# Kernel optimization log

Hardware: AMD Instinct MI355X
Metric: run time of the kernel (lower is better)

The kernel has to match this reference:

```python
import jax, jax.numpy as jnp
import numpy as np

B, G, D_EMB = 4096, 20000, 512
H_LOW, N_HIDDEN = 512, 1024
TOPK, T, FILM_W = 64, 0.1, 1.0
LN_EPS = 1e-5


def _layer_norm(x, gamma, beta):
    mu = jnp.mean(x, axis=-1, keepdims=True)
    var = jnp.mean(jnp.square(x - mu), axis=-1, keepdims=True)
    return (x - mu) * jax.lax.rsqrt(var + LN_EPS) * gamma + beta


def _l2norm(x, eps=1e-12):
    n = jnp.sqrt(jnp.sum(jnp.square(x), axis=-1, keepdims=True))
    return x / jnp.maximum(n, eps)


def setup_inputs() -> dict:
    key = jax.random.key(0)
    ks = jax.random.split(key, 8)
    s = 0.02
    return {
        "x": jax.random.normal(ks[0], (B, G), jnp.float32),
        "g": jax.random.normal(ks[1], (G, D_EMB), jnp.float32),
        "W_enc": jax.random.normal(ks[2], (H_LOW, G), jnp.float32) * s,
        "b_enc": jnp.zeros((H_LOW,), jnp.float32),
        "ln1_g": jnp.ones((H_LOW,), jnp.float32),
        "ln1_b": jnp.zeros((H_LOW,), jnp.float32),
        "W_ga": jax.random.normal(ks[3], (H_LOW, D_EMB), jnp.float32) * s,
        "W_gamma": jax.random.normal(ks[4], (H_LOW, H_LOW), jnp.float32) * s,
        "b_gamma": jnp.zeros((H_LOW,), jnp.float32),
        "W_beta": jax.random.normal(ks[5], (H_LOW, H_LOW), jnp.float32) * s,
        "b_beta": jnp.zeros((H_LOW,), jnp.float32),
        "W_exp": jax.random.normal(ks[6], (N_HIDDEN, H_LOW), jnp.float32) * s,
        "b_exp": jnp.zeros((N_HIDDEN,), jnp.float32),
        "ln2_g": jnp.ones((N_HIDDEN,), jnp.float32),
        "ln2_b": jnp.zeros((N_HIDDEN,), jnp.float32),
    }


def reference(x, g, W_enc, b_enc, ln1_g, ln1_b, W_ga, W_gamma, b_gamma,
              W_beta, b_beta, W_exp, b_exp, ln2_g, ln2_b):
    # x_encoder: Linear -> LayerNorm -> GELU (dropout = eval no-op)
    h = jnp.dot(x, W_enc.T) + b_enc                    # [B, H_LOW]
    h = jax.nn.gelu(_layer_norm(h, ln1_g, ln1_b), approximate=False)
    # gene adapter + cosine scores
    e = _l2norm(jnp.dot(g, W_ga.T))                    # [G, H_LOW]
    h_x = _l2norm(h)                                   # [B, H_LOW]
    scores = jnp.dot(h_x, e.T) / T                     # [B, G]
    # top-k mask + masked softmax attention
    _, idx = jax.lax.top_k(scores, TOPK)               # [B, TOPK]
    mask = jnp.zeros_like(scores).at[jnp.arange(B)[:, None], idx].set(1.0)
    attn = jax.nn.softmax(jnp.where(mask == 0, -1e9, scores), axis=-1)
    ctx = jnp.dot(attn, e)                             # [B, H_LOW]
    # FiLM (identity-centered)
    gamma = (jnp.dot(ctx, W_gamma.T) + b_gamma) * FILM_W
    beta = (jnp.dot(ctx, W_beta.T) + b_beta) * FILM_W
    h_cell = (1.0 + gamma) * h_x + beta
    # x_expand: Linear -> LayerNorm -> GELU
    h2 = jnp.dot(h_cell, W_exp.T) + b_exp              # [B, N_HIDDEN]
    return jax.nn.gelu(_layer_norm(h2, ln2_g, ln2_b), approximate=False)
```

## Files before the change

### kernel.cpp

```cpp
#include <hip/hip_runtime.h>
#include <hip/hip_fp16.h>
#include <math.h>
#include <type_traits>

#define DEVI __device__ __forceinline__

typedef __attribute__((ext_vector_type(8))) short bf16x8;
typedef __attribute__((ext_vector_type(4))) float f32x4;
typedef __attribute__((ext_vector_type(4))) unsigned int u32x4;
typedef unsigned short ushort_t;

DEVI unsigned int pack_bf16(float a, float b) {
  unsigned int ua = __float_as_uint(a), ub = __float_as_uint(b);
  ua = (ua + 0x7FFFu + ((ua >> 16) & 1u)) >> 16;
  ub = (ub + 0x7FFFu + ((ub >> 16) & 1u)) >> 16;
  return ua | (ub << 16);
}

DEVI ushort_t rnd_bf16(float a) {
  unsigned int ua = __float_as_uint(a);
  return (ushort_t)((ua + 0x7FFFu + ((ua >> 16) & 1u)) >> 16);
}

DEVI bf16x8 cvt_bf16x8(f32x4 lo, f32x4 hi) {
  unsigned int r0, r1, r2, r3;
  asm("v_cvt_pk_bf16_f32 %0, %1, %2" : "=v"(r0) : "v"(lo[0]), "v"(lo[1]));
  asm("v_cvt_pk_bf16_f32 %0, %1, %2" : "=v"(r1) : "v"(lo[2]), "v"(lo[3]));
  asm("v_cvt_pk_bf16_f32 %0, %1, %2" : "=v"(r2) : "v"(hi[0]), "v"(hi[1]));
  asm("v_cvt_pk_bf16_f32 %0, %1, %2" : "=v"(r3) : "v"(hi[2]), "v"(hi[3]));
  union { u32x4 u; bf16x8 v; } x;
  x.u = u32x4{r0, r1, r2, r3};
  return x.v;
}

template<int SPLITZ, bool TAIL>
__global__ __launch_bounds__(512, 1) void bgemmA32(
    const float* __restrict__ A, const ushort_t* __restrict__ B,
    float* __restrict__ C, int M, int N, int K, int nbn, int nbm)
{
  __shared__ __align__(16) char L[131072];
  const int tid = threadIdx.x, lane = tid & 63, wv = tid >> 6;

  const int nwg = gridDim.x;
  const int hw = blockIdx.x;
  const int q = nwg >> 3, r = nwg & 7;
  const int xcd = hw & 7, pos = hw >> 3;
  const int lid = (xcd < r ? xcd * (q + 1) : r * (q + 1) + (xcd - r) * q) + pos;
  const int bn = lid % nbn;
  const int t2 = lid / nbn;
  const int bm = t2 % nbm;
  const int z  = t2 / nbm;

  const int ksteps = K >> 6;
  const int szk = (ksteps + SPLITZ - 1) / SPLITZ;
  const int kbBeg = z * szk;
  const int kbEnd = min(ksteps, kbBeg + szk);

  const int wm = wv >> 2, wn = wv & 3;
  const int lrow = lane & 15, kg = lane >> 4;

  f32x4 acc[4][4];
#pragma unroll
  for (int i = 0; i < 4; ++i)
#pragma unroll
    for (int j = 0; j < 4; ++j) acc[i][j] = f32x4{0.f, 0.f, 0.f, 0.f};

  const int alr = lane >> 3, ag32 = (lane & 7) >> 1;
  const float* aS[2];
#pragma unroll
  for (int j = 0; j < 2; ++j) {
    const int lr = (wv * 2 + j) * 8 + alr;
    const int swz = (lr ^ (lr >> 2)) & 3;
    const int colf = ((ag32 ^ swz) << 3) + (lane & 1) * 4;
    aS[j] = A + (size_t)min(bm * 128 + lr, M - 1) * (size_t)K + colf;
  }
  const int blr = lane >> 2, bgq = lane & 3;
  const ushort_t* bS[2];
#pragma unroll
  for (int j = 0; j < 2; ++j) {
    const int lr = (wv * 2 + j) * 16 + blr;
    const int swz = (lr ^ (lr >> 2)) & 3;
    bS[j] = B + (size_t)min(bn * 256 + lr, N - 1) * (size_t)K + ((bgq ^ swz) << 3);
  }

  int offA[4], offB[4];
#pragma unroll
  for (int i = 0; i < 4; ++i) {
    const int ra = wm * 64 + i * 16 + lrow;
    offA[i] = ra * 128 + ((kg ^ ((ra ^ (ra >> 2)) & 3)) << 5);
  }
#pragma unroll
  for (int j = 0; j < 4; ++j) {
    const int rb = wn * 64 + j * 16 + lrow;
    offB[j] = rb * 64 + ((kg ^ ((rb ^ (rb >> 2)) & 3)) << 4);
  }

#define GA_STGA(h, k0v) do {                                                  \
    _Pragma("unroll")                                                         \
    for (int j_ = 0; j_ < 2; ++j_)                                            \
      __builtin_amdgcn_global_load_lds(                                       \
          (const __attribute__((address_space(1))) void*)(aS[j_] + (k0v) + (h) * 32), \
          (__attribute__((address_space(3))) void*)                           \
              (L + (s ^ 1) * 32768 + (h) * 16384 + (wv * 2 + j_) * 1024),     \
          16, 0, 0);                                                          \
  } while (0)
#define GA_STGB(h, k0v) do {                                                  \
    _Pragma("unroll")                                                         \
    for (int j_ = 0; j_ < 2; ++j_)                                            \
      __builtin_amdgcn_global_load_lds(                                       \
          (const __attribute__((address_space(1))) void*)(bS[j_] + (k0v) + (h) * 32), \
          (__attribute__((address_space(3))) void*)                           \
              (L + 65536 + (s ^ 1) * 32768 + (h) * 16384 + (wv * 2 + j_) * 1024), \
          16, 0, 0);                                                          \
  } while (0)
#define GA_RDB(h) do {                                                        \
    _Pragma("unroll")                                                         \
    for (int j_ = 0; j_ < 4; ++j_)                                            \
      bfv[j_] = *(const bf16x8*)(L + 65536 + s * 32768 + (h) * 16384 + offB[j_]); \
  } while (0)
#define GA_RDA(h, rg) do {                                                    \
    _Pragma("unroll")                                                         \
    for (int i_ = 0; i_ < 2; ++i_) {                                          \
      const char* pa_ = L + s * 32768 + (h) * 16384 + offA[(rg) * 2 + i_];    \
      af[i_] = cvt_bf16x8(*(const f32x4*)pa_, *(const f32x4*)(pa_ + 16));     \
    }                                                                         \
  } while (0)
#define GA_MM(rg) do {                                                        \
    _Pragma("unroll")                                                         \
    for (int i_ = 0; i_ < 2; ++i_)                                            \
      _Pragma("unroll")                                                       \
      for (int j_ = 0; j_ < 4; ++j_)                                          \
        acc[(rg) * 2 + i_][j_] = __builtin_amdgcn_mfma_f32_16x16x32_bf16(     \
            af[i_], bfv[j_], acc[(rg) * 2 + i_][j_], 0, 0, 0);                \
  } while (0)
#define GA_BAR asm volatile("s_barrier" ::: "memory")

  {
    int s = 1;
    const int k0 = kbBeg << 6;
    GA_STGA(0, k0); GA_STGB(0, k0); GA_STGA(1, k0); GA_STGB(1, k0);
  }
  asm volatile("s_waitcnt vmcnt(4)" ::: "memory");
  GA_BAR;

  int s = 0;
  for (int t = kbBeg; t < kbEnd; ++t) {
    const bool more = (t + 1 < kbEnd);
    const int k0n = (t + 1) << 6;
    bf16x8 af[2], bfv[4];
    GA_RDB(0); GA_RDA(0, 0);
    if (more) GA_STGA(0, k0n);
    GA_BAR;
    __builtin_amdgcn_s_setprio(1); GA_MM(0); __builtin_amdgcn_s_setprio(0);
    GA_BAR;
    GA_RDA(0, 1);
    if (more) GA_STGB(0, k0n);
    GA_BAR;
    __builtin_amdgcn_s_setprio(1); GA_MM(1); __builtin_amdgcn_s_setprio(0);
    if (more) asm volatile("s_waitcnt vmcnt(4)" ::: "memory");
    else      asm volatile("s_waitcnt vmcnt(0)" ::: "memory");
    GA_BAR;
    GA_RDB(1); GA_RDA(1, 0);
    if (more) GA_STGA(1, k0n);
    GA_BAR;
    __builtin_amdgcn_s_setprio(1); GA_MM(0); __builtin_amdgcn_s_setprio(0);
    GA_BAR;
    GA_RDA(1, 1);
    if (more) GA_STGB(1, k0n);
    GA_BAR;
    __builtin_amdgcn_s_setprio(1); GA_MM(1); __builtin_amdgcn_s_setprio(0);
    if (more) asm volatile("s_waitcnt vmcnt(4)" ::: "memory");
    GA_BAR;
    s ^= 1;
  }

  if (TAIL && z == SPLITZ - 1 && (K & 63)) {
    const int k0t = ksteps << 6;
    bf16x8 af[2], bfv[4];
#pragma unroll
    for (int j = 0; j < 2; ++j) {
      const float4 av = *(const float4*)(aS[j] + k0t);
      *(float4*)(L + s * 32768 + (wv * 2 + j) * 1024 + lane * 16) = av;
      const u32x4 bv = *(const u32x4*)(bS[j] + k0t);
      *(u32x4*)(L + 65536 + s * 32768 + (wv * 2 + j) * 1024 + lane * 16) = bv;
    }
    __syncthreads();
    GA_RDB(0);
    GA_RDA(0, 0); GA_MM(0);
    GA_RDA(0, 1); GA_MM(1);
  }
#undef GA_STGA
#undef GA_STGB
#undef GA_RDB
#undef GA_RDA
#undef GA_MM
#undef GA_BAR

  const size_t zoff = (SPLITZ > 1) ? (size_t)z * (size_t)M * (size_t)N : 0;
#pragma unroll
  for (int i = 0; i < 4; ++i) {
#pragma unroll
    for (int j = 0; j < 4; ++j) {
      const int col = bn * 256 + wn * 64 + j * 16 + lrow;
      if (col >= N) continue;
      const int row0 = bm * 128 + wm * 64 + i * 16 + kg * 4;
#pragma unroll
      for (int rr = 0; rr < 4; ++rr) {
        const int gr = row0 + rr;
        if (gr < M) C[zoff + (size_t)gr * (size_t)N + col] = acc[i][j][rr];
      }
    }
  }
}

template<int SPLITZ, typename OutT>
__global__ __launch_bounds__(512, 1) void bgemm256(
    const ushort_t* __restrict__ A, const ushort_t* __restrict__ B,
    OutT* __restrict__ C, int M, int N, int K, int nbn, int nbm)
{
  __shared__ __align__(16) char L[131072];
  const int tid = threadIdx.x, lane = tid & 63, wv = tid >> 6;

  const int nwg = gridDim.x;
  const int hw = blockIdx.x;
  const int q = nwg >> 3, r = nwg & 7;
  const int xcd = hw & 7, pos = hw >> 3;
  const int lid = (xcd < r ? xcd * (q + 1) : r * (q + 1) + (xcd - r) * q) + pos;
  const int bn = lid % nbn;
  const int t2 = lid / nbn;
  const int bm = t2 % nbm;
  const int z  = t2 / nbm;

  const int ksteps = K >> 6;
  int kbBeg = 0, kbEnd = ksteps;
  if (SPLITZ > 1) {
    const int sz = (ksteps + SPLITZ - 1) / SPLITZ;
    kbBeg = z * sz;
    kbEnd = min(ksteps, kbBeg + sz);
  }

  const int wm = wv >> 2, wn = wv & 3;
  const int lrow = lane & 15, kg = lane >> 4;

  f32x4 acc[8][4];
#pragma unroll
  for (int i = 0; i < 8; ++i)
#pragma unroll
    for (int j = 0; j < 4; ++j) acc[i][j] = f32x4{0.f, 0.f, 0.f, 0.f};

  const int sr = lane >> 2, sq = lane & 3;
  const ushort_t* aS[2];
  const ushort_t* bS[2];
#pragma unroll
  for (int j = 0; j < 2; ++j) {
    const int lr = (wv * 2 + j) * 16 + sr;
    const int swz = (lr ^ (lr >> 2)) & 3;
    aS[j] = A + (size_t)min(bm * 256 + lr, M - 1) * (size_t)K + ((sq ^ swz) << 3);
    bS[j] = B + (size_t)min(bn * 256 + lr, N - 1) * (size_t)K + ((sq ^ swz) << 3);
  }

  int offA[8], offB[4];
#pragma unroll
  for (int i = 0; i < 8; ++i) {
    const int ra = wm * 128 + i * 16 + lrow;
    offA[i] = ra * 64 + (((kg ^ ((ra ^ (ra >> 2)) & 3))) << 4);
  }
#pragma unroll
  for (int j = 0; j < 4; ++j) {
    const int rb = wn * 64 + j * 16 + lrow;
    offB[j] = rb * 64 + (((kg ^ ((rb ^ (rb >> 2)) & 3))) << 4);
  }

#define G256_STG(isB, h, k0v) do {                                            \
    _Pragma("unroll")                                                         \
    for (int j_ = 0; j_ < 2; ++j_)                                            \
      __builtin_amdgcn_global_load_lds(                                       \
          (const __attribute__((address_space(1))) void*)                     \
              (((isB) ? bS : aS)[j_] + (k0v) + (h) * 32),                     \
          (__attribute__((address_space(3))) void*)                           \
              (L + (isB) * 65536 + (s ^ 1) * 32768 + (h) * 16384 +            \
               (wv * 2 + j_) * 1024), 16, 0, 0);                              \
  } while (0)
#define G256_RDA(h, rg) do {                                                  \
    _Pragma("unroll")                                                         \
    for (int i_ = 0; i_ < 4; ++i_)                                            \
      af[i_] = *(const bf16x8*)(L + s * 32768 + (h) * 16384 +                 \
                                offA[(rg) * 4 + i_]);                         \
  } while (0)
#define G256_RDB(h) do {                                                      \
    _Pragma("unroll")                                                         \
    for (int j_ = 0; j_ < 4; ++j_)                                            \
      bfv[j_] = *(const bf16x8*)(L + 65536 + s * 32768 + (h) * 16384 +        \
                                 offB[j_]);                                   \
  } while (0)
#define G256_MM(rg) do {                                                      \
    _Pragma("unroll")                                                         \
    for (int i_ = 0; i_ < 4; ++i_)                                            \
      _Pragma("unroll")                                                       \
      for (int j_ = 0; j_ < 4; ++j_)                                          \
        acc[(rg) * 4 + i_][j_] = __builtin_amdgcn_mfma_f32_16x16x32_bf16(     \
            af[i_], bfv[j_], acc[(rg) * 4 + i_][j_], 0, 0, 0);                \
  } while (0)
#define G256_BAR asm volatile("s_barrier" ::: "memory")

  {
    int s = 1;
    const int k0 = kbBeg << 6;
    G256_STG(0, 0, k0);
    G256_STG(1, 0, k0);
    G256_STG(0, 1, k0);
    G256_STG(1, 1, k0);
  }
  asm volatile("s_waitcnt vmcnt(4)" ::: "memory");
  G256_BAR;

  int s = 0;
  for (int t = kbBeg; t < kbEnd; ++t) {
    const bool more = (t + 1 < kbEnd);
    const int k0n = (t + 1) << 6;
    bf16x8 af[4], bfv[4];
    G256_RDB(0);
    G256_RDA(0, 0);
    if (more) G256_STG(0, 0, k0n);
    G256_BAR;
    __builtin_amdgcn_s_setprio(1); G256_MM(0); __builtin_amdgcn_s_setprio(0);
    G256_BAR;
    G256_RDA(0, 1);
    if (more) G256_STG(1, 0, k0n);
    G256_BAR;
    __builtin_amdgcn_s_setprio(1); G256_MM(1); __builtin_amdgcn_s_setprio(0);
    if (more) asm volatile("s_waitcnt vmcnt(4)" ::: "memory");
    else      asm volatile("s_waitcnt vmcnt(0)" ::: "memory");
    G256_BAR;
    G256_RDB(1);
    G256_RDA(1, 0);
    if (more) G256_STG(0, 1, k0n);
    G256_BAR;
    __builtin_amdgcn_s_setprio(1); G256_MM(0); __builtin_amdgcn_s_setprio(0);
    G256_BAR;
    G256_RDA(1, 1);
    if (more) G256_STG(1, 1, k0n);
    G256_BAR;
    __builtin_amdgcn_s_setprio(1); G256_MM(1); __builtin_amdgcn_s_setprio(0);
    if (more) asm volatile("s_waitcnt vmcnt(4)" ::: "memory");
    G256_BAR;
    s ^= 1;
  }
#undef G256_STG
#undef G256_RDA
#undef G256_RDB
#undef G256_MM
#undef G256_BAR

  const size_t zoff = (SPLITZ > 1) ? (size_t)z * (size_t)M * (size_t)N : 0;
#pragma unroll
  for (int i = 0; i < 8; ++i) {
#pragma unroll
    for (int j = 0; j < 4; ++j) {
      const int col = bn * 256 + wn * 64 + j * 16 + lrow;
      if (col >= N) continue;
      const int row0 = bm * 256 + wm * 128 + i * 16 + kg * 4;
#pragma unroll
      for (int rr = 0; rr < 4; ++rr) {
        const int gr = row0 + rr;
        if (gr < M) {
          const float v = acc[i][j][rr];
          if constexpr (std::is_same<OutT, __half>::value)
            C[zoff + (size_t)gr * (size_t)N + col] = __float2half(v);
          else
            C[zoff + (size_t)gr * (size_t)N + col] = v;
        }
      }
    }
  }
}

template<typename AT, int SPLITZ, bool BIAS, typename OutT>
__global__ __launch_bounds__(512, sizeof(AT) == 2 ? 3 : 2) void bgemm(
    const AT* __restrict__ A, const ushort_t* __restrict__ B0,
    const float* __restrict__ bias0, OutT* __restrict__ C,
    int M, int N, int K, int nbn, int nbm)
{
  constexpr bool AB16 = (sizeof(AT) == 2);
  __shared__ __align__(16) char AsB[AB16 ? 16384 : 32768];
  __shared__ __align__(16) char BsB[32768];
  const int tid = threadIdx.x, lane = tid & 63, wv = tid >> 6;

  const int nwg = gridDim.x;
  const int hw = blockIdx.x;
  const int q = nwg >> 3, r = nwg & 7;
  const int xcd = hw & 7, pos = hw >> 3;
  const int lid = (xcd < r ? xcd * (q + 1) : r * (q + 1) + (xcd - r) * q) + pos;
  const int bn = lid % nbn;
  const int t2 = lid / nbn;
  const int bm = t2 % nbm;
  const int z  = t2 / nbm;

  const ushort_t* B  = B0;
  const float* bias  = bias0;

  const int ksteps = (K + 63) >> 6;
  int kbBeg = 0, kbEnd = ksteps;
  if (SPLITZ > 1) {
    const int sz = (ksteps + SPLITZ - 1) / SPLITZ;
    kbBeg = z * sz;
    kbEnd = min(ksteps, kbBeg + sz);
  }

  const int wr = (wv >> 2) * 64;
  const int wc = (wv & 3) * 64;
  const int lrow = lane & 15, kg = lane >> 4;

  f32x4 acc[4][4];
#pragma unroll
  for (int i = 0; i < 4; ++i)
#pragma unroll
    for (int j = 0; j < 4; ++j) acc[i][j] = f32x4{0.f, 0.f, 0.f, 0.f};

  const AT* aSrc[4];
  if constexpr (AB16) {
    const int r0 = lane >> 3;
    const int ce = ((lane & 7) ^ r0) << 3;
#pragma unroll
    for (int j = 0; j < 2; ++j) {
      const int row = wv * 16 + j * 8 + r0;
      aSrc[j] = A + (size_t)min(bm * 128 + row, M - 1) * (size_t)K + ce;
    }
  } else {
    const int r0 = lane >> 4;
#pragma unroll
    for (int j = 0; j < 4; ++j) {
      const int row = wv * 16 + j * 4 + r0;
      const int ca = ((lane & 15) << 2) ^ ((row & 7) << 3);
      aSrc[j] = A + (size_t)min(bm * 128 + row, M - 1) * (size_t)K + ca;
    }
  }
  const int rB0 = lane >> 3;
  const int colB = ((lane & 7) ^ rB0) << 3;
  const ushort_t* bSrc[4];
#pragma unroll
  for (int j = 0; j < 4; ++j) {
    const int row = wv * 32 + j * 8 + rB0;
    bSrc[j] = B + (size_t)min(bn * 256 + row, N - 1) * (size_t)K + colB;
  }

  for (int kb = kbBeg; kb < kbEnd; ++kb) {
    const int k0 = kb << 6;
    if constexpr (AB16) {
#pragma unroll
      for (int j = 0; j < 2; ++j)
        __builtin_amdgcn_global_load_lds(
            (const __attribute__((address_space(1))) void*)(aSrc[j] + k0),
            (__attribute__((address_space(3))) void*)(AsB + (wv * 2 + j) * 1024),
            16, 0, 0);
    } else {
#pragma unroll
      for (int j = 0; j < 4; ++j)
        __builtin_amdgcn_global_load_lds(
            (const __attribute__((address_space(1))) void*)(aSrc[j] + k0),
            (__attribute__((address_space(3))) void*)(AsB + (wv * 4 + j) * 1024),
            16, 0, 0);
    }
#pragma unroll
    for (int j = 0; j < 4; ++j)
      __builtin_amdgcn_global_load_lds(
          (const __attribute__((address_space(1))) void*)(bSrc[j] + k0),
          (__attribute__((address_space(3))) void*)(BsB + (wv * 4 + j) * 1024),
          16, 0, 0);
    __syncthreads();
#pragma unroll
    for (int kk = 0; kk < 2; ++kk) {
      bf16x8 af[4], bfr[4];
#pragma unroll
      for (int i = 0; i < 4; ++i) {
        const int ra = wr + i * 16 + lrow;
        if constexpr (AB16) {
          af[i] = *(const bf16x8*)(AsB + ra * 128 + ((((kk << 2) + kg) ^ (ra & 7)) << 4));
        } else {
          const char* pa = AsB + ra * 256 + ((kk * 128 + (kg << 5)) ^ ((ra & 7) << 5));
          af[i] = cvt_bf16x8(*(const f32x4*)pa, *(const f32x4*)(pa + 16));
        }
        const int rb = wc + i * 16 + lrow;
        bfr[i] = *(const bf16x8*)(BsB + rb * 128 + ((((kk << 2) + kg) ^ (rb & 7)) << 4));
      }
#pragma unroll
      for (int i = 0; i < 4; ++i)
#pragma unroll
        for (int j = 0; j < 4; ++j)
          acc[i][j] = __builtin_amdgcn_mfma_f32_16x16x32_bf16(af[i], bfr[j], acc[i][j], 0, 0, 0);
    }
    __syncthreads();
  }

  const size_t zoff = (SPLITZ > 1) ? (size_t)z * (size_t)M * (size_t)N : 0;
#pragma unroll
  for (int i = 0; i < 4; ++i) {
#pragma unroll
    for (int j = 0; j < 4; ++j) {
      const int col = bn * 256 + wc + j * 16 + lrow;
      if (col >= N) continue;
      const int row0 = bm * 128 + wr + i * 16 + kg * 4;
      float bv = 0.f;
      if (BIAS) bv = bias[col];
#pragma unroll
      for (int rr = 0; rr < 4; ++rr) {
        const int gr = row0 + rr;
        if (gr < M) {
          const float v = acc[i][j][rr] + bv;
          if constexpr (std::is_same<OutT, __half>::value)
            C[zoff + (size_t)gr * (size_t)N + col] = __float2half(v);
          else
            C[zoff + (size_t)gr * (size_t)N + col] = v;
        }
      }
    }
  }
}

__global__ __launch_bounds__(512, 2) void bgemm_film(
    const ushort_t* __restrict__ A, const ushort_t* __restrict__ BG,
    const ushort_t* __restrict__ BB, const float* __restrict__ bg,
    const float* __restrict__ bb, const float* __restrict__ hx,
    ushort_t* __restrict__ hcb)
{
  constexpr int M = 4096, N = 512, K = 512;
  __shared__ __align__(16) char AsB[16384];
  __shared__ __align__(16) char BsB[65536];
  const int tid = threadIdx.x, lane = tid & 63, wv = tid >> 6;

  const int nwg = gridDim.x;
  const int hw = blockIdx.x;
  const int q = nwg >> 3, r = nwg & 7;
  const int xcd = hw & 7, pos = hw >> 3;
  const int lid = (xcd < r ? xcd * (q + 1) : r * (q + 1) + (xcd - r) * q) + pos;
  const int bn = lid % 2;
  const int bm = lid / 2;

  const int wr = (wv >> 2) * 64;
  const int wc = (wv & 3) * 64;
  const int lrow = lane & 15, kg = lane >> 4;

  f32x4 accG[4][4], accB[4][4];
#pragma unroll
  for (int i = 0; i < 4; ++i)
#pragma unroll
    for (int j = 0; j < 4; ++j) {
      accG[i][j] = f32x4{0.f, 0.f, 0.f, 0.f};
      accB[i][j] = f32x4{0.f, 0.f, 0.f, 0.f};
    }

  const int r0 = lane >> 3;
  const int ce = ((lane & 7) ^ r0) << 3;
  const ushort_t* aSrc[2];
#pragma unroll
  for (int j = 0; j < 2; ++j) {
    const int row = wv * 16 + j * 8 + r0;
    aSrc[j] = A + (size_t)(bm * 128 + row) * (size_t)K + ce;
  }
  const ushort_t* gSrc[4];
  const ushort_t* bSrc[4];
#pragma unroll
  for (int j = 0; j < 4; ++j) {
    const int row = wv * 32 + j * 8 + r0;
    gSrc[j] = BG + (size_t)(bn * 256 + row) * (size_t)K + ce;
    bSrc[j] = BB + (size_t)(bn * 256 + row) * (size_t)K + ce;
  }

  for (int kb = 0; kb < K / 64; ++kb) {
    const int k0 = kb << 6;
#pragma unroll
    for (int j = 0; j < 2; ++j)
      __builtin_amdgcn_global_load_lds(
          (const __attribute__((address_space(1))) void*)(aSrc[j] + k0),
          (__attribute__((address_space(3))) void*)(AsB + (wv * 2 + j) * 1024),
          16, 0, 0);
#pragma unroll
    for (int j = 0; j < 4; ++j) {
      __builtin_amdgcn_global_load_lds(
          (const __attribute__((address_space(1))) void*)(gSrc[j] + k0),
          (__attribute__((address_space(3))) void*)(BsB + (wv * 4 + j) * 1024),
          16, 0, 0);
      __builtin_amdgcn_global_load_lds(
          (const __attribute__((address_space(1))) void*)(bSrc[j] + k0),
          (__attribute__((address_space(3))) void*)(BsB + 32768 + (wv * 4 + j) * 1024),
          16, 0, 0);
    }
    __syncthreads();
#pragma unroll
    for (int kk = 0; kk < 2; ++kk) {
      bf16x8 af[4], bfG[4], bfB[4];
#pragma unroll
      for (int i = 0; i < 4; ++i) {
        const int ra = wr + i * 16 + lrow;
        af[i] = *(const bf16x8*)(AsB + ra * 128 + ((((kk << 2) + kg) ^ (ra & 7)) << 4));
        const int rb = wc + i * 16 + lrow;
        const int bo = rb * 128 + ((((kk << 2) + kg) ^ (rb & 7)) << 4);
        bfG[i] = *(const bf16x8*)(BsB + bo);
        bfB[i] = *(const bf16x8*)(BsB + 32768 + bo);
      }
#pragma unroll
      for (int i = 0; i < 4; ++i)
#pragma unroll
        for (int j = 0; j < 4; ++j) {
          accG[i][j] = __builtin_amdgcn_mfma_f32_16x16x32_bf16(af[i], bfG[j], accG[i][j], 0, 0, 0);
          accB[i][j] = __builtin_amdgcn_mfma_f32_16x16x32_bf16(af[i], bfB[j], accB[i][j], 0, 0, 0);
        }
    }
    __syncthreads();
  }

#pragma unroll
  for (int i = 0; i < 4; ++i) {
#pragma unroll
    for (int j = 0; j < 4; ++j) {
      const int col = bn * 256 + wc + j * 16 + lrow;
      const float gvb = bg[col], bvb = bb[col];
      const int row0 = bm * 128 + wr + i * 16 + kg * 4;
#pragma unroll
      for (int rr = 0; rr < 4; ++rr) {
        const int gr = row0 + rr;
        const float gm = accG[i][j][rr] + gvb;
        const float bt = accB[i][j][rr] + bvb;
        const float h = hx[(size_t)gr * N + col];
        hcb[(size_t)gr * N + col] = rnd_bf16((1.f + gm) * h + bt);
      }
    }
  }
}

__global__ __launch_bounds__(256) void f2b(
    const float4* __restrict__ in, u32x4* __restrict__ out, int n8)
{
  const int i = blockIdx.x * 256 + threadIdx.x;
  if (i < n8) {
    const float4 a = in[2 * i], b = in[2 * i + 1];
    u32x4 o = { pack_bf16(a.x, a.y), pack_bf16(a.z, a.w),
                pack_bf16(b.x, b.y), pack_bf16(b.z, b.w) };
    out[i] = o;
  }
}

__global__ __launch_bounds__(256) void gee_fuse_ln1(
    const float* __restrict__ P, const float* __restrict__ b_enc,
    const float* __restrict__ g1, const float* __restrict__ b1,
    float* __restrict__ hx, unsigned int* __restrict__ hxb)
{
  const int row = blockIdx.x, tid = threadIdx.x;
  __shared__ float red[16];
  const size_t MN = (size_t)4096 * 512;
  const size_t o2 = (size_t)row * 256 + tid;
  float2 v = ((const float2*)b_enc)[tid];
#pragma unroll
  for (int qq = 0; qq < 4; ++qq) {
    const float2 p = ((const float2*)P)[qq * (MN / 2) + o2];
    v.x += p.x; v.y += p.y;
  }
  float a = v.x + v.y;
  float b = v.x * v.x + v.y * v.y;
#pragma unroll
  for (int o = 32; o > 0; o >>= 1) { a += __shfl_xor(a, o); b += __shfl_xor(b, o); }
  const int lane = tid & 63, wvi = tid >> 6;
  if (lane == 0) { red[wvi] = a; red[8 + wvi] = b; }
  __syncthreads();
  const float mu  = (red[0] + red[1] + red[2] + red[3]) * (1.f / 512.f);
  const float ex2 = (red[8] + red[9] + red[10] + red[11]) * (1.f / 512.f);
  const float inv = rsqrtf(ex2 - mu * mu + 1e-5f);
  const float2 gg = ((const float2*)g1)[tid];
  const float2 bb = ((const float2*)b1)[tid];
  const float y0 = (v.x - mu) * inv * gg.x + bb.x;
  const float y1 = (v.y - mu) * inv * gg.y + bb.y;
  const float t0 = 0.5f * y0 * (1.f + erff(y0 * 0.70710678118654752f));
  const float t1 = 0.5f * y1 * (1.f + erff(y1 * 0.70710678118654752f));
  float ss = t0 * t0 + t1 * t1;
  __syncthreads();
#pragma unroll
  for (int o = 32; o > 0; o >>= 1) ss += __shfl_xor(ss, o);
  if (lane == 0) red[wvi] = ss;
  __syncthreads();
  const float sc = 1.f / fmaxf(sqrtf(red[0] + red[1] + red[2] + red[3]), 1e-12f);
  const float h0 = t0 * sc, h1 = t1 * sc;
  ((float2*)hx)[o2] = make_float2(h0, h1);
  hxb[o2] = pack_bf16(h0, h1);
}

__global__ __launch_bounds__(256) void gee_l2rows(
    const __half2* __restrict__ ein, unsigned int* __restrict__ eb)
{
  const int row = blockIdx.x, tid = threadIdx.x;
  __shared__ float red[4];
  const __half2 h = ein[(size_t)row * 256 + tid];
  const float vx = __half2float(h.x), vy = __half2float(h.y);
  float ss = vx * vx + vy * vy;
#pragma unroll
  for (int o = 32; o > 0; o >>= 1) ss += __shfl_xor(ss, o);
  if ((tid & 63) == 0) red[tid >> 6] = ss;
  __syncthreads();
  const float sc = 1.f / fmaxf(sqrtf(red[0] + red[1] + red[2] + red[3]), 1e-12f);
  eb[(size_t)row * 256 + tid] = pack_bf16(vx * sc, vy * sc);
}

__global__ __launch_bounds__(256) void gee_topk_ctx(
    const __half* __restrict__ scores, const unsigned int* __restrict__ eb,
    unsigned int* __restrict__ ctxb)
{
  constexpr int G = 20000, GQ = G / 8, CAP = 2048, TCAP = 160;
  constexpr unsigned int SPEC = 0xADu;
  const int row = blockIdx.x, tid = threadIdx.x;
  const int lane = tid & 63, wv = tid >> 6;
  __shared__ int hist[4][256];
  __shared__ int cnt_ge[256];
  __shared__ int wtop[4];
  __shared__ unsigned int comp[CAP];
  __shared__ int whist[4][16];
  __shared__ int sel[64];
  __shared__ float swt[64];
  __shared__ int tie[TCAP];
  __shared__ int s_thr, s_above, s_cand, s_cnt, s_n1, s_n2;

  const u32x4* srow128 = (const u32x4*)((const ushort_t*)scores + (size_t)row * G);
  const ushort_t* srow16 = (const ushort_t*)srow128;

#pragma unroll
  for (int b = 0; b < 4; ++b) hist[b][tid] = 0;
  if (tid == 0) { s_cnt = 0; s_n1 = 0; s_n2 = 0; }
  __syncthreads();

  for (int j0 = 0; j0 < GQ; j0 += 256) {
    const int j = j0 + tid;
    if (j < GQ) {
      const u32x4 pv = srow128[j];
#pragma unroll
      for (int c = 0; c < 4; ++c) {
        const unsigned int p = pv[c];
        const unsigned int f = (((p >> 15) & 0x10001u) * 0x7FFFu) + 0x80008000u;
        const unsigned int k2 = p ^ f;
        const unsigned int bl = (k2 >> 8) & 0xFFu, bh = k2 >> 24;
        atomicAdd(&hist[wv][bl], 1);
        atomicAdd(&hist[wv][bh], 1);
        if (bl >= SPEC) {
          const int pp = atomicAdd(&s_cnt, 1);
          if (pp < CAP) comp[pp] = ((k2 & 0xFFFFu) << 16) | (unsigned)(8 * j + 2 * c);
        }
        if (bh >= SPEC) {
          const int pp = atomicAdd(&s_cnt, 1);
          if (pp < CAP) comp[pp] = ((k2 >> 16) << 16) | (unsigned)(8 * j + 2 * c + 1);
        }
      }
    }
  }
  __syncthreads();
  cnt_ge[tid] = hist[0][tid] + hist[1][tid] + hist[2][tid] + hist[3][tid];
  __syncthreads();
  for (int off = 1; off < 256; off <<= 1) {
    const int add = (tid + off < 256) ? cnt_ge[tid + off] : 0;
    __syncthreads();
    cnt_ge[tid] += add;
    __syncthreads();
  }
  {
    const unsigned long long m = __ballot(cnt_ge[tid] >= 64);
    if (lane == 0) wtop[wv] = m ? (wv * 64 + 63 - __clzll(m)) : -1;
  }
  __syncthreads();
  if (tid == 0) {
    const int thrB = max(max(wtop[0], wtop[1]), max(wtop[2], wtop[3]));
    s_cand  = cnt_ge[thrB];
    s_above = (thrB == 255) ? 0 : cnt_ge[thrB + 1];
    s_thr   = thrB << 8;
  }
  __syncthreads();

  const unsigned int thrB = ((unsigned int)s_thr) >> 8;
  const int specCnt = cnt_ge[SPEC];
  const bool useSpec = (thrB >= SPEC) && (specCnt <= CAP);
  const bool useComp = useSpec || (s_cand <= CAP);

  if (!useSpec && useComp) {
    __syncthreads();
    if (tid == 0) s_cnt = 0;
    __syncthreads();
    for (int j0 = 0; j0 < GQ; j0 += 256) {
      const int j = j0 + tid;
      if (j < GQ) {
        const u32x4 pv = srow128[j];
#pragma unroll
        for (int c = 0; c < 4; ++c) {
          const unsigned int p = pv[c];
          const unsigned int f = (((p >> 15) & 0x10001u) * 0x7FFFu) + 0x80008000u;
          const unsigned int k2 = p ^ f;
          const unsigned int lo = k2 & 0xFFFFu, hi = k2 >> 16;
          if ((lo >> 8) >= thrB) {
            const int pp = atomicAdd(&s_cnt, 1);
            comp[pp] = (lo << 16) | (unsigned)(8 * j + 2 * c);
          }
          if ((hi >> 8) >= thrB) {
            const int pp = atomicAdd(&s_cnt, 1);
            comp[pp] = (hi << 16) | (unsigned)(8 * j + 2 * c + 1);
          }
        }
      }
    }
  }
  __syncthreads();
  const int Nloop = useComp ? min(s_cnt, CAP) : G;

  for (int pass = 2; pass < 4; ++pass) {
    const int shift = 12 - 4 * pass;
    const unsigned int thr = (unsigned int)s_thr;
    const unsigned int pfx = thr >> (shift + 4);
    int c[16];
#pragma unroll
    for (int b = 0; b < 16; ++b) c[b] = 0;
    for (int j0 = 0; j0 < Nloop; j0 += 256) {
      const int j = j0 + tid;
      const bool ok = j < Nloop;
      unsigned int key;
      if (useComp) {
        key = ok ? (comp[j] >> 16) : 0u;
      } else {
        const unsigned int raw = ok ? (unsigned int)srow16[j] : 0u;
        key = (raw & 0x8000u) ? (0xFFFFu & ~raw) : (raw | 0x8000u);
      }
      const unsigned int nb = (ok && (key >> (shift + 4)) == pfx) ? ((key >> shift) & 15u) : 0xFFu;
#pragma unroll
      for (int b = 0; b < 16; ++b) c[b] += __popcll(__ballot(nb == (unsigned)b));
    }
    if (lane == 0) {
#pragma unroll
      for (int b = 0; b < 16; ++b) whist[wv][b] = c[b];
    }
    __syncthreads();
    if (tid == 0) {
      int run = s_above;
      for (int vv = 15; vv >= 0; --vv) {
        const int c4 = whist[0][vv] + whist[1][vv] + whist[2][vv] + whist[3][vv];
        if (run + c4 >= 64) { s_thr |= vv << shift; break; }
        run += c4;
      }
      s_above = run;
    }
    __syncthreads();
  }

  const unsigned int kthr = (unsigned int)s_thr;
  for (int j0 = 0; j0 < Nloop; j0 += 256) {
    const int j = j0 + tid;
    if (j < Nloop) {
      unsigned int key, idx;
      if (useComp) {
        const unsigned int u = comp[j];
        key = u >> 16; idx = u & 0xFFFFu;
      } else {
        const unsigned int raw = (unsigned int)srow16[j];
        key = (raw & 0x8000u) ? (0xFFFFu & ~raw) : (raw | 0x8000u);
        idx = (unsigned)j;
      }
      if (key > kthr) {
        const int pp = atomicAdd(&s_n1, 1);
        sel[pp] = (int)idx;
      } else if (key == kthr) {
        const int pp = atomicAdd(&s_n2, 1);
        if (pp < TCAP) tie[pp] = (int)idx;
      }
    }
  }
  __syncthreads();
  if (tid == 0) {
    const int n1 = s_n1;
    const int n2 = min(s_n2, TCAP);
    const int need = 64 - n1;
    for (int rr = 0; rr < need; ++rr) {
      int best = 1 << 30, bj = 0;
      for (int j = 0; j < n2; ++j)
        if (tie[j] < best) { best = tie[j]; bj = j; }
      sel[n1 + rr] = best;
      tie[bj] = 1 << 30;
    }
  }
  __syncthreads();
  if (tid < 64) {
    const int idx = sel[tid];
    const float sv = __half2float(scores[(size_t)row * G + idx]) * 10.0f;
    float m = sv;
#pragma unroll
    for (int o = 32; o > 0; o >>= 1) m = fmaxf(m, __shfl_xor(m, o));
    const float w = __expf(sv - m);
    float d = w;
#pragma unroll
    for (int o = 32; o > 0; o >>= 1) d += __shfl_xor(d, o);
    swt[tid] = w / d;
  }
  __syncthreads();
  float a0 = 0.f, a1 = 0.f;
#pragma unroll 4
  for (int k = 0; k < 64; ++k) {
    const unsigned int pk = eb[(size_t)sel[k] * 256 + tid];
    const float wk = swt[k];
    a0 += wk * __uint_as_float(pk << 16);
    a1 += wk * __uint_as_float(pk & 0xFFFF0000u);
  }
  ctxb[(size_t)row * 256 + tid] = pack_bf16(a0, a1);
}

__global__ __launch_bounds__(256) void gee_ln2(
    const float* __restrict__ h2, const float* __restrict__ g2,
    const float* __restrict__ b2, float* __restrict__ out)
{
  const int row = blockIdx.x, tid = threadIdx.x;
  __shared__ float red[16];
  float v[4];
  float a = 0.f, b = 0.f;
#pragma unroll
  for (int e = 0; e < 4; ++e) {
    v[e] = h2[(size_t)row * 1024 + tid + e * 256];
    a += v[e]; b += v[e] * v[e];
  }
#pragma unroll
  for (int o = 32; o > 0; o >>= 1) { a += __shfl_xor(a, o); b += __shfl_xor(b, o); }
  const int lane = tid & 63, wvi = tid >> 6;
  if (lane == 0) { red[wvi] = a; red[8 + wvi] = b; }
  __syncthreads();
  const float mu  = (red[0] + red[1] + red[2] + red[3]) * (1.f / 1024.f);
  const float ex2 = (red[8] + red[9] + red[10] + red[11]) * (1.f / 1024.f);
  const float inv = rsqrtf(ex2 - mu * mu + 1e-5f);
#pragma unroll
  for (int e = 0; e < 4; ++e) {
    const int c = tid + e * 256;
    const float y = (v[e] - mu) * inv * g2[c] + b2[c];
    out[(size_t)row * 1024 + c] = 0.5f * y * (1.f + erff(y * 0.70710678118654752f));
  }
}

extern "C" void kernel_launch(void* const* d_in, const int* in_sizes, int n_in,
                              void* d_out, int out_size, void* d_ws, size_t ws_size,
                              hipStream_t stream)
{
  const float* x       = (const float*)d_in[0];
  const float* g       = (const float*)d_in[1];
  const float* W_enc   = (const float*)d_in[2];
  const float* b_enc   = (const float*)d_in[3];
  const float* ln1_g   = (const float*)d_in[4];
  const float* ln1_b   = (const float*)d_in[5];
  const float* W_ga    = (const float*)d_in[6];
  const float* W_gamma = (const float*)d_in[7];
  const float* b_gamma = (const float*)d_in[8];
  const float* W_beta  = (const float*)d_in[9];
  const float* b_beta  = (const float*)d_in[10];
  const float* W_exp   = (const float*)d_in[11];
  const float* b_exp   = (const float*)d_in[12];
  const float* ln2_g   = (const float*)d_in[13];
  const float* ln2_b   = (const float*)d_in[14];
  float* out = (float*)d_out;

  char* ws = (char*)d_ws;
  constexpr size_t OFF_SCORES = 0;
  constexpr size_t OFF_H2     = 0;
  constexpr size_t OFF_PART   = 163840000;
  constexpr size_t OFF_WENCB  = 197394432;
  constexpr size_t OFF_E      = 197394432;
  constexpr size_t OFF_EB     = 217874432;
  constexpr size_t OFF_HX     = 238354432;
  constexpr size_t OFF_HXB    = 246743040;
  constexpr size_t OFF_CTXB   = 250937344;
  constexpr size_t OFF_HCB    = 255131648;
  constexpr size_t OFF_WGAB   = 259325952;
  constexpr size_t OFF_WGMB   = 259850240;
  constexpr size_t OFF_WBTB   = 260374528;
  constexpr size_t OFF_WEXB   = 260898816;

  __half*       scores = (__half*)(ws + OFF_SCORES);
  float*        h2     = (float*)(ws + OFF_H2);
  float*        part   = (float*)(ws + OFF_PART);
  ushort_t*     wencb  = (ushort_t*)(ws + OFF_WENCB);
  __half*       e      = (__half*)(ws + OFF_E);
  unsigned int* eb     = (unsigned int*)(ws + OFF_EB);
  float*        hx     = (float*)(ws + OFF_HX);
  unsigned int* hxb    = (unsigned int*)(ws + OFF_HXB);
  unsigned int* ctxb   = (unsigned int*)(ws + OFF_CTXB);
  ushort_t*     hcb    = (ushort_t*)(ws + OFF_HCB);
  ushort_t*     wgab   = (ushort_t*)(ws + OFF_WGAB);
  ushort_t*     wgmb   = (ushort_t*)(ws + OFF_WGMB);
  ushort_t*     wbtb   = (ushort_t*)(ws + OFF_WBTB);
  ushort_t*     wexb   = (ushort_t*)(ws + OFF_WEXB);

  f2b<<<5000, 256, 0, stream>>>((const float4*)W_enc,   (u32x4*)wencb, 1280000);
  f2b<<<128,  256, 0, stream>>>((const float4*)W_ga,    (u32x4*)wgab,  32768);
  f2b<<<128,  256, 0, stream>>>((const float4*)W_gamma, (u32x4*)wgmb,  32768);
  f2b<<<128,  256, 0, stream>>>((const float4*)W_beta,  (u32x4*)wbtb,  32768);
  f2b<<<256,  256, 0, stream>>>((const float4*)W_exp,   (u32x4*)wexb,  65536);

  bgemmA32<4, true><<<256, 512, 0, stream>>>(
      x, wencb, part, 4096, 512, 20000, 2, 32);
  gee_fuse_ln1<<<4096, 256, 0, stream>>>(part, b_enc, ln1_g, ln1_b, hx, hxb);
  bgemm<float, 1, false, __half><<<314, 512, 0, stream>>>(
      g, wgab, nullptr, e, 20000, 512, 512, 2, 157);
  gee_l2rows<<<20000, 256, 0, stream>>>((const __half2*)e, eb);
  bgemm256<1, __half><<<1264, 512, 0, stream>>>(
      (const ushort_t*)hxb, (const ushort_t*)eb, scores, 4096, 20000, 512, 79, 16);
  gee_topk_ctx<<<4096, 256, 0, stream>>>(scores, eb, ctxb);
  bgemm_film<<<64, 512, 0, stream>>>(
      (const ushort_t*)ctxb, wgmb, wbtb, b_gamma, b_beta, hx, hcb);
  bgemm<ushort_t, 1, true, float><<<128, 512, 0, stream>>>(
      hcb, wexb, b_exp, h2, 4096, 1024, 512, 4, 32);
  gee_ln2<<<4096, 256, 0, stream>>>(h2, ln2_g, ln2_b, out);
}
```

Measured before the change: 481.5 us.

## Emit top-k candidates from score GEMM epilogue to skip full-row scans

The scores GEMM epilogue now tests each fp16 score against a fixed speculative key threshold and appends qualifying (key, column) pairs to a per-row global candidate list with a global atomic counter. The top-k kernel loads that list directly when its count lies between 64 and 2048, skipping the full-row histogram and compaction scans over 20000 scores and starting radix refinement from pass 0. Otherwise it falls back to the old histogram path. The cost is global atomics and scattered writes in the GEMM epilogue, plus an extra memset.

```diff
diff --git a/kernel.cpp b/kernel.cpp
--- a/kernel.cpp
+++ b/kernel.cpp
@@ -213,10 +213,11 @@
   }
 }
 
-template<int SPLITZ, typename OutT>
+template<int SPLITZ, typename OutT, bool CANDF>
 __global__ __launch_bounds__(512, 1) void bgemm256(
     const ushort_t* __restrict__ A, const ushort_t* __restrict__ B,
-    OutT* __restrict__ C, int M, int N, int K, int nbn, int nbm)
+    OutT* __restrict__ C, unsigned int* __restrict__ cand,
+    int* __restrict__ cand_cnt, int M, int N, int K, int nbn, int nbm)
 {
   __shared__ __align__(16) char L[131072];
   const int tid = threadIdx.x, lane = tid & 63, wv = tid >> 6;
@@ -365,10 +366,22 @@
         const int gr = row0 + rr;
         if (gr < M) {
           const float v = acc[i][j][rr];
-          if constexpr (std::is_same<OutT, __half>::value)
-            C[zoff + (size_t)gr * (size_t)N + col] = __float2half(v);
-          else
+          if constexpr (std::is_same<OutT, __half>::value) {
+            const __half hv = __float2half(v);
+            C[zoff + (size_t)gr * (size_t)N + col] = hv;
+            if constexpr (CANDF) {
+              const unsigned int raw = (unsigned int)__half_as_ushort(hv);
+              const unsigned int key =
+                  (raw & 0x8000u) ? ((~raw) & 0xFFFFu) : (raw | 0x8000u);
+              if ((key >> 8) >= 0xADu) {
+                const int pp = atomicAdd(&cand_cnt[gr], 1);
+                if (pp < 2048)
+                  cand[(size_t)gr * 2048 + pp] = (key << 16) | (unsigned)col;
+              }
+            }
+          } else {
             C[zoff + (size_t)gr * (size_t)N + col] = v;
+          }
         }
       }
     }
@@ -701,10 +714,10 @@
 
 __global__ __launch_bounds__(256) void gee_topk_ctx(
     const __half* __restrict__ scores, const unsigned int* __restrict__ eb,
+    const unsigned int* __restrict__ cand, const int* __restrict__ cand_cnt,
     unsigned int* __restrict__ ctxb)
 {
   constexpr int G = 20000, GQ = G / 8, CAP = 2048, TCAP = 160;
-  constexpr unsigned int SPEC = 0xADu;
   const int row = blockIdx.x, tid = threadIdx.x;
   const int lane = tid & 63, wv = tid >> 6;
   __shared__ int hist[4][256];
@@ -720,64 +733,26 @@
   const u32x4* srow128 = (const u32x4*)((const ushort_t*)scores + (size_t)row * G);
   const ushort_t* srow16 = (const ushort_t*)srow128;
 
-#pragma unroll
-  for (int b = 0; b < 4; ++b) hist[b][tid] = 0;
-  if (tid == 0) { s_cnt = 0; s_n1 = 0; s_n2 = 0; }
+  const int gcnt = cand_cnt[row];
+  const bool fast = (gcnt >= 64 && gcnt <= CAP);
+
+  if (tid == 0) { s_cnt = 0; s_n1 = 0; s_n2 = 0; s_thr = 0; s_above = 0; }
   __syncthreads();
 
-  for (int j0 = 0; j0 < GQ; j0 += 256) {
-    const int j = j0 + tid;
-    if (j < GQ) {
-      const u32x4 pv = srow128[j];
-#pragma unroll
-      for (int c = 0; c < 4; ++c) {
-        const unsigned int p = pv[c];
-        const unsigned int f = (((p >> 15) & 0x10001u) * 0x7FFFu) + 0x80008000u;
-        const unsigned int k2 = p ^ f;
-        const unsigned int bl = (k2 >> 8) & 0xFFu, bh = k2 >> 24;
-        atomicAdd(&hist[wv][bl], 1);
-        atomicAdd(&hist[wv][bh], 1);
-        if (bl >= SPEC) {
-          const int pp = atomicAdd(&s_cnt, 1);
-          if (pp < CAP) comp[pp] = ((k2 & 0xFFFFu) << 16) | (unsigned)(8 * j + 2 * c);
-        }
-        if (bh >= SPEC) {
-          const int pp = atomicAdd(&s_cnt, 1);
-          if (pp < CAP) comp[pp] = ((k2 >> 16) << 16) | (unsigned)(8 * j + 2 * c + 1);
-        }
-      }
-    }
-  }
-  __syncthreads();
-  cnt_ge[tid] = hist[0][tid] + hist[1][tid] + hist[2][tid] + hist[3][tid];
-  __syncthreads();
-  for (int off = 1; off < 256; off <<= 1) {
-    const int add = (tid + off < 256) ? cnt_ge[tid + off] : 0;
-    __syncthreads();
-    cnt_ge[tid] += add;
-    __syncthreads();
-  }
-  {
-    const unsigned long long m = __ballot(cnt_ge[tid] >= 64);
-    if (lane == 0) wtop[wv] = m ? (wv * 64 + 63 - __clzll(m)) : -1;
-  }
-  __syncthreads();
-  if (tid == 0) {
-    const int thrB = max(max(wtop[0], wtop[1]), max(wtop[2], wtop[3]));
-    s_cand  = cnt_ge[thrB];
-    s_above = (thrB == 255) ? 0 : cnt_ge[thrB + 1];
-    s_thr   = thrB << 8;
-  }
-  __syncthreads();
-
-  const unsigned int thrB = ((unsigned int)s_thr) >> 8;
-  const int specCnt = cnt_ge[SPEC];
-  const bool useSpec = (thrB >= SPEC) && (specCnt <= CAP);
-  const bool useComp = useSpec || (s_cand <= CAP);
-
-  if (!useSpec && useComp) {
-    __syncthreads();
-    if (tid == 0) s_cnt = 0;
+  int passBeg;
+  bool useComp;
+  int Nloop;
+
+  if (fast) {
+    for (int j = tid; j < gcnt; j += 256)
+      comp[j] = cand[(size_t)row * CAP + j];
+    passBeg = 0;
+    useComp = true;
+    Nloop = gcnt;
+    __syncthreads();
+  } else {
+#pragma unroll
+    for (int b = 0; b < 4; ++b) hist[b][tid] = 0;
     __syncthreads();
     for (int j0 = 0; j0 < GQ; j0 += 256) {
       const int j = j0 + tid;
@@ -788,23 +763,63 @@
           const unsigned int p = pv[c];
           const unsigned int f = (((p >> 15) & 0x10001u) * 0x7FFFu) + 0x80008000u;
           const unsigned int k2 = p ^ f;
-          const unsigned int lo = k2 & 0xFFFFu, hi = k2 >> 16;
-          if ((lo >> 8) >= thrB) {
-            const int pp = atomicAdd(&s_cnt, 1);
-            comp[pp] = (lo << 16) | (unsigned)(8 * j + 2 * c);
-          }
-          if ((hi >> 8) >= thrB) {
-            const int pp = atomicAdd(&s_cnt, 1);
-            comp[pp] = (hi << 16) | (unsigned)(8 * j + 2 * c + 1);
+          atomicAdd(&hist[wv][(k2 >> 8) & 0xFFu], 1);
+          atomicAdd(&hist[wv][k2 >> 24], 1);
+        }
+      }
+    }
+    __syncthreads();
+    cnt_ge[tid] = hist[0][tid] + hist[1][tid] + hist[2][tid] + hist[3][tid];
+    __syncthreads();
+    for (int off = 1; off < 256; off <<= 1) {
+      const int add = (tid + off < 256) ? cnt_ge[tid + off] : 0;
+      __syncthreads();
+      cnt_ge[tid] += add;
+      __syncthreads();
+    }
+    {
+      const unsigned long long m = __ballot(cnt_ge[tid] >= 64);
+      if (lane == 0) wtop[wv] = m ? (wv * 64 + 63 - __clzll(m)) : -1;
+    }
+    __syncthreads();
+    if (tid == 0) {
+      const int thrB = max(max(wtop[0], wtop[1]), max(wtop[2], wtop[3]));
+      s_cand  = cnt_ge[thrB];
+      s_above = (thrB == 255) ? 0 : cnt_ge[thrB + 1];
+      s_thr   = thrB << 8;
+    }
+    __syncthreads();
+    const unsigned int thrB = ((unsigned int)s_thr) >> 8;
+    useComp = (s_cand <= CAP);
+    if (useComp) {
+      for (int j0 = 0; j0 < GQ; j0 += 256) {
+        const int j = j0 + tid;
+        if (j < GQ) {
+          const u32x4 pv = srow128[j];
+#pragma unroll
+          for (int c = 0; c < 4; ++c) {
+            const unsigned int p = pv[c];
+            const unsigned int f = (((p >> 15) & 0x10001u) * 0x7FFFu) + 0x80008000u;
+            const unsigned int k2 = p ^ f;
+            const unsigned int lo = k2 & 0xFFFFu, hi = k2 >> 16;
+            if ((lo >> 8) >= thrB) {
+              const int pp = atomicAdd(&s_cnt, 1);
+              comp[pp] = (lo << 16) | (unsigned)(8 * j + 2 * c);
+            }
+            if ((hi >> 8) >= thrB) {
+              const int pp = atomicAdd(&s_cnt, 1);
+              comp[pp] = (hi << 16) | (unsigned)(8 * j + 2 * c + 1);
+            }
           }
         }
       }
     }
-  }
-  __syncthreads();
-  const int Nloop = useComp ? min(s_cnt, CAP) : G;
-
-  for (int pass = 2; pass < 4; ++pass) {
+    __syncthreads();
+    passBeg = 2;
+    Nloop = useComp ? s_cnt : G;
+  }
+
+  for (int pass = passBeg; pass < 4; ++pass) {
     const int shift = 12 - 4 * pass;
     const unsigned int thr = (unsigned int)s_thr;
     const unsigned int pfx = thr >> (shift + 4);
@@ -967,6 +982,8 @@
   constexpr size_t OFF_WGMB   = 259850240;
   constexpr size_t OFF_WBTB   = 260374528;
   constexpr size_t OFF_WEXB   = 260898816;
+  constexpr size_t OFF_CAND   = 261947392;
+  constexpr size_t OFF_CCNT   = 295501824;
 
   __half*       scores = (__half*)(ws + OFF_SCORES);
   float*        h2     = (float*)(ws + OFF_H2);
@@ -982,7 +999,10 @@
   ushort_t*     wgmb   = (ushort_t*)(ws + OFF_WGMB);
   ushort_t*     wbtb   = (ushort_t*)(ws + OFF_WBTB);
   ushort_t*     wexb   = (ushort_t*)(ws + OFF_WEXB);
-
+  unsigned int* cand   = (unsigned int*)(ws + OFF_CAND);
+  int*          ccnt   = (int*)(ws + OFF_CCNT);
+
+  hipMemsetAsync(ccnt, 0, 4096 * sizeof(int), stream);
   f2b<<<5000, 256, 0, stream>>>((const float4*)W_enc,   (u32x4*)wencb, 1280000);
   f2b<<<128,  256, 0, stream>>>((const float4*)W_ga,    (u32x4*)wgab,  32768);
   f2b<<<128,  256, 0, stream>>>((const float4*)W_gamma, (u32x4*)wgmb,  32768);
@@ -995,9 +1015,10 @@
   bgemm<float, 1, false, __half><<<314, 512, 0, stream>>>(
       g, wgab, nullptr, e, 20000, 512, 512, 2, 157);
   gee_l2rows<<<20000, 256, 0, stream>>>((const __half2*)e, eb);
-  bgemm256<1, __half><<<1264, 512, 0, stream>>>(
-      (const ushort_t*)hxb, (const ushort_t*)eb, scores, 4096, 20000, 512, 79, 16);
-  gee_topk_ctx<<<4096, 256, 0, stream>>>(scores, eb, ctxb);
+  bgemm256<1, __half, true><<<1264, 512, 0, stream>>>(
+      (const ushort_t*)hxb, (const ushort_t*)eb, scores, cand, ccnt,
+      4096, 20000, 512, 79, 16);
+  gee_topk_ctx<<<4096, 256, 0, stream>>>(scores, eb, cand, ccnt, ctxb);
   bgemm_film<<<64, 512, 0, stream>>>(
       (const ushort_t*)ctxb, wgmb, wbtb, b_gamma, b_beta, hx, hcb);
   bgemm<ushort_t, 1, true, float><<<128, 512, 0, stream>>>(
```

After: 1.238 ms. 2.57x slower.
